# Performance work log

Measured on AMD Instinct MI355X. Metric: run time of the kernel, lower is better.

The kernel has to match this reference:

```python
import jax, jax.numpy as jnp
import numpy as np

N_EMBD = 512
HEAD_SIZE = 64
B, T = 256, 256


def setup_inputs() -> dict:
    key = jax.random.key(0)
    ks = jax.random.split(key, 7)
    s = 1.0 / np.sqrt(N_EMBD)
    return {
        "x": jax.random.normal(ks[0], (B, T, N_EMBD), dtype=jnp.float32),
        "Wk": jax.random.uniform(ks[1], (N_EMBD, HEAD_SIZE), jnp.float32, -s, s),
        "bk": jax.random.uniform(ks[2], (HEAD_SIZE,), jnp.float32, -s, s),
        "Wq": jax.random.uniform(ks[3], (N_EMBD, HEAD_SIZE), jnp.float32, -s, s),
        "bq": jax.random.uniform(ks[4], (HEAD_SIZE,), jnp.float32, -s, s),
        "Wv": jax.random.uniform(ks[5], (N_EMBD, HEAD_SIZE), jnp.float32, -s, s),
        "bv": jax.random.uniform(ks[6], (HEAD_SIZE,), jnp.float32, -s, s),
    }


def reference(x, Wk, bk, Wq, bq, Wv, bv):
    # Single-head causal self-attention (dropout = identity in eval mode).
    Bq, Tq, C = x.shape
    k = x @ Wk + bk        # [B, T, H]
    q = x @ Wq + bq        # [B, T, H]
    v = x @ Wv + bv        # [B, T, H]
    scale = 1.0 / jnp.sqrt(jnp.asarray(k.shape[-1], x.dtype))
    scores = jnp.einsum('bth,bsh->bts', q, k) * scale  # [B, T, T]
    causal = jnp.tril(jnp.ones((Tq, Tq), dtype=bool))
    scores = jnp.where(causal, scores, -jnp.inf)
    attn = jax.nn.softmax(scores, axis=-1)
    return jnp.einsum('bts,bsh->bth', attn, v)  # [B, T, H]
```

## Files before the change

kernel.cpp:

```cpp
#include <hip/hip_runtime.h>
#include <stdint.h>

typedef __attribute__((ext_vector_type(8))) short bf16x8;
typedef __attribute__((ext_vector_type(4))) float f32x4;

#if __has_builtin(__builtin_amdgcn_exp2f)
#define EXP2F(x) __builtin_amdgcn_exp2f(x)
#else
#define EXP2F(x) exp2f(x)
#endif

__device__ __forceinline__ short f2bf(float f) {
    union { float f; uint32_t u; } c; c.f = f;
    return (short)((c.u + 0x7fffu + ((c.u >> 16) & 1u)) >> 16);
}

typedef __attribute__((address_space(1))) void gvoid;
typedef __attribute__((address_space(3))) void lvoid;
__device__ __forceinline__ void async_cp16(const void* g, void* l) {
    __builtin_amdgcn_global_load_lds((gvoid*)g, (lvoid*)l, 16, 0, 0);
}

__global__ void prep_kernel(const float* __restrict__ Wk, const float* __restrict__ bk,
                            const float* __restrict__ Wq, const float* __restrict__ bq,
                            const float* __restrict__ Wv, const float* __restrict__ bv,
                            short* __restrict__ Wt2g, float* __restrict__ bcat) {
    const int col = blockIdx.x;
    const float* W; const float* bb; int c0;
    if (col < 64)       { W = Wk; bb = bk; c0 = col; }
    else if (col < 128) { W = Wq; bb = bq; c0 = col - 64; }
    else                { W = Wv; bb = bv; c0 = col - 128; }
    for (int c = threadIdx.x; c < 512; c += blockDim.x) {
        const int k5 = c & 31;
        Wt2g[(c >> 5) * 6144 + col * 32 + ((((k5 >> 3) ^ (col & 3)) << 3)) + (k5 & 7)] =
            f2bf(W[(size_t)c * 64 + c0]);
    }
    if (threadIdx.x == 0) bcat[col] = bb[c0];
}

#define PSTR 40

__global__ __launch_bounds__(1024, 4) void fused_kernel(
    const float* __restrict__ x, const short* __restrict__ Wt2g,
    const float* __restrict__ bcat, float* __restrict__ out) {
    extern __shared__ __align__(16) char smem[];

    const int tid = threadIdx.x;
    const int wave = tid >> 6, lane = tid & 63;
    const int quad = lane >> 4, l16 = lane & 15;
    const int b = blockIdx.x;
    const int t = wave;

    f32x4 acc[12];
#pragma unroll
    for (int i = 0; i < 12; i++) acc[i] = (f32x4){0.f, 0.f, 0.f, 0.f};

    const int xr = lane >> 3;
    const int xsl = lane & 7;

#define STAGE_X(kc, bufp)                                                           \
    for (int g = 0; g < 2; g++) {                                                   \
        const int i = wave + g * 16;                                                \
        const int r = i * 8 + xr;                                                   \
        const int s = xsl ^ ((r & 3) << 1);                                         \
        async_cp16(x + ((size_t)b * 256 + r) * 512 + (kc) * 32 + s * 4,             \
                   smem + (bufp) * 32768 + i * 1024);                               \
    }
#define STAGE_W(kc, bufp)                                                           \
    if (wave < 12) {                                                                \
        async_cp16(Wt2g + (size_t)(kc) * 6144 + wave * 512 + lane * 8,              \
                   smem + 65536 + (bufp) * 12288 + wave * 1024);                    \
    }

    STAGE_X(0, 0)
    STAGE_W(0, 0)
    __syncthreads();

    const int axoff = (quad ^ (l16 & 3)) * 8;
    const int bxoff = (quad ^ (l16 & 3)) << 3;
    const int arow = t * 16 + l16;
    for (int kc = 0; kc < 16; kc++) {
        const int buf = kc & 1;
        if (kc < 15) { STAGE_X(kc + 1, buf ^ 1) STAGE_W(kc + 1, buf ^ 1) }
        const float* xa = (const float*)(smem + buf * 32768) + arow * 32 + axoff;
        f32x4 u0 = *(const f32x4*)xa, u1 = *(const f32x4*)(xa + 4);
        bf16x8 a;
#pragma unroll
        for (int i = 0; i < 4; i++) { a[i] = f2bf(u0[i]); a[4 + i] = f2bf(u1[i]); }
        const short* wb = (const short*)(smem + 65536 + buf * 12288);
#pragma unroll
        for (int nt = 0; nt < 12; nt++) {
            bf16x8 bfrag = *(const bf16x8*)&wb[(nt * 16 + l16) * 32 + bxoff];
            acc[nt] = __builtin_amdgcn_mfma_f32_16x16x32_bf16(a, bfrag, acc[nt], 0, 0, 0);
        }
        __syncthreads();
    }

    short* Ks  = (short*)smem;
    short* Qs  = (short*)(smem + 32768);
    short* Vts = (short*)(smem + 65536);
    short* Ps  = (short*)(smem + 98304);
#pragma unroll
    for (int nt = 0; nt < 12; nt++) {
        const int col = nt * 16 + l16;
        const float bias = bcat[col];
        const int h = col & 63;
#pragma unroll
        for (int r = 0; r < 4; r++) {
            const short v = f2bf(acc[nt][r] + bias);
            const int row = t * 16 + quad * 4 + r;
            if (nt < 4)
                Ks[row * 64 + (((h >> 3) ^ (row & 7)) << 3) + (h & 7)] = v;
            else if (nt < 8)
                Qs[row * 64 + (((h >> 3) ^ (row & 7)) << 3) + (h & 7)] = v;
            else
                Vts[h * 256 + (((row >> 3) ^ (h & 7)) << 3) + (row & 7)] = v;
        }
    }
    __syncthreads();

    const int qt = ((wave >> 2) << 2) | ((wave & 3) ^ (wave >> 2));
    const float sc2 = 0.125f * 1.44269504088896340736f;
    short* myP = Ps + wave * (16 * PSTR);

    const int qrow = qt * 16 + l16;
    const int sw = l16 & 7;
    bf16x8 qf0 = *(const bf16x8*)&Qs[qrow * 64 + ((quad ^ sw) << 3)];
    bf16x8 qf1 = *(const bf16x8*)&Qs[qrow * 64 + (((4 + quad) ^ sw) << 3)];

    f32x4 St[16];
#pragma unroll
    for (int i = 0; i < 16; i++) St[i] = (f32x4){0.f, 0.f, 0.f, 0.f};
    __builtin_amdgcn_s_setprio(1);
#pragma unroll
    for (int nt = 0; nt < 16; nt++) if (nt <= qt) {
        const int krow = nt * 16 + l16;
        bf16x8 kf0 = *(const bf16x8*)&Ks[krow * 64 + ((quad ^ sw) << 3)];
        bf16x8 kf1 = *(const bf16x8*)&Ks[krow * 64 + (((4 + quad) ^ sw) << 3)];
        St[nt] = __builtin_amdgcn_mfma_f32_16x16x32_bf16(qf0, kf0, St[nt], 0, 0, 0);
        St[nt] = __builtin_amdgcn_mfma_f32_16x16x32_bf16(qf1, kf1, St[nt], 0, 0, 0);
    }
    __builtin_amdgcn_s_setprio(0);

    const int rowq = qt * 16 + quad * 4;
    float mx[4], ls[4];
#pragma unroll
    for (int r = 0; r < 4; r++) mx[r] = -3.0e38f;
#pragma unroll
    for (int nt = 0; nt < 16; nt++) if (nt <= qt) {
        const int cs = nt * 16 + l16;
#pragma unroll
        for (int r = 0; r < 4; r++) {
            float s = (cs <= rowq + r) ? St[nt][r] * sc2 : -3.0e38f;
            St[nt][r] = s;
            mx[r] = fmaxf(mx[r], s);
        }
    }
#pragma unroll
    for (int d = 1; d < 16; d <<= 1)
#pragma unroll
        for (int r = 0; r < 4; r++)
            mx[r] = fmaxf(mx[r], __shfl_xor(mx[r], d, 64));
#pragma unroll
    for (int r = 0; r < 4; r++) ls[r] = 0.f;
#pragma unroll
    for (int nt = 0; nt < 16; nt++) if (nt <= qt) {
#pragma unroll
        for (int r = 0; r < 4; r++) {
            float p = EXP2F(St[nt][r] - mx[r]);
            St[nt][r] = p;
            ls[r] += p;
        }
    }
#pragma unroll
    for (int d = 1; d < 16; d <<= 1)
#pragma unroll
        for (int r = 0; r < 4; r++)
            ls[r] += __shfl_xor(ls[r], d, 64);

    f32x4 O[4];
#pragma unroll
    for (int i = 0; i < 4; i++) O[i] = (f32x4){0.f, 0.f, 0.f, 0.f};
    const int nch = (qt + 2) >> 1;
    __builtin_amdgcn_s_setprio(1);
#pragma unroll
    for (int c2 = 0; c2 < 8; c2++) if (c2 < nch) {
#pragma unroll
        for (int t2i = 0; t2i < 2; t2i++) {
            const int nt = c2 * 2 + t2i;
#pragma unroll
            for (int r = 0; r < 4; r++)
                myP[(quad * 4 + r) * PSTR + t2i * 16 + l16] = f2bf(St[nt][r]);
        }
        bf16x8 pf = *(const bf16x8*)&myP[l16 * PSTR + quad * 8];
#pragma unroll
        for (int ht = 0; ht < 4; ht++) {
            const int h = ht * 16 + l16;
            bf16x8 vf = *(const bf16x8*)&Vts[h * 256 + (((c2 * 4 + quad) ^ (h & 7)) << 3)];
            O[ht] = __builtin_amdgcn_mfma_f32_16x16x32_bf16(pf, vf, O[ht], 0, 0, 0);
        }
    }
    __builtin_amdgcn_s_setprio(0);

    float rls[4];
#pragma unroll
    for (int r = 0; r < 4; r++) rls[r] = 1.0f / ls[r];
#pragma unroll
    for (int ht = 0; ht < 4; ht++)
#pragma unroll
        for (int r = 0; r < 4; r++)
            out[((size_t)b * 256 + rowq + r) * 64 + ht * 16 + l16] = O[ht][r] * rls[r];
#undef STAGE_X
#undef STAGE_W
}

extern "C" void kernel_launch(void* const* d_in, const int* in_sizes, int n_in,
                              void* d_out, int out_size, void* d_ws, size_t ws_size,
                              hipStream_t stream) {
    const float* x  = (const float*)d_in[0];
    const float* Wk = (const float*)d_in[1];
    const float* bk = (const float*)d_in[2];
    const float* Wq = (const float*)d_in[3];
    const float* bq = (const float*)d_in[4];
    const float* Wv = (const float*)d_in[5];
    const float* bv = (const float*)d_in[6];
    float* out = (float*)d_out;

    char* ws = (char*)d_ws;
    short* Wt2g = (short*)(ws);
    float* bcat = (float*)(ws + 196608);

    const int smem_bytes = 118784;
    (void)hipFuncSetAttribute((const void*)fused_kernel,
                              hipFuncAttributeMaxDynamicSharedMemorySize, smem_bytes);

    prep_kernel<<<192, 256, 0, stream>>>(Wk, bk, Wq, bq, Wv, bv, Wt2g, bcat);
    fused_kernel<<<256, 1024, smem_bytes, stream>>>(x, Wt2g, bcat, out);
}
```

Baseline: 217.3 us.

## Split fused projection+attention into separate projection and attention kernels

Moves the QKV projection out of the fused per-batch kernel into its own kernel with 1024 blocks of 256 threads, each handling 64 rows. The projection writes bf16 K, Q and V (V pre-transposed, in the swizzled layout) to a workspace, and the attention kernel bulk-loads them into LDS asynchronously. This aims to raise occupancy and parallelism during the projection GEMM, which previously ran with only 256 large blocks. The cost is an extra global round-trip of about 25 MB of intermediate K/Q/V and one more kernel launch.

```diff
diff --git a/kernel.cpp b/kernel.cpp
--- a/kernel.cpp
+++ b/kernel.cpp
@@ -38,86 +38,125 @@
     if (threadIdx.x == 0) bcat[col] = bb[c0];
 }
 
+__global__ __launch_bounds__(256, 4) void proj_kernel(
+    const float* __restrict__ x, const short* __restrict__ Wt2g,
+    const float* __restrict__ bcat, short* __restrict__ kqv) {
+    __shared__ __align__(16) char smem[40960];
+
+    const int tid = threadIdx.x;
+    const int wave = tid >> 6, lane = tid & 63;
+    const int quad = lane >> 4, l16 = lane & 15;
+    const int blk = blockIdx.x;
+    const int b = blk >> 2, rt = blk & 3;
+    const size_t grow0 = (size_t)blk * 64;
+
+    f32x4 acc[12];
+#pragma unroll
+    for (int i = 0; i < 12; i++) acc[i] = (f32x4){0.f, 0.f, 0.f, 0.f};
+
+    const int xr = lane >> 3;
+    const int xsl = lane & 7;
+
+#define STAGE_X(kc, bufp)                                                           \
+    for (int g = 0; g < 2; g++) {                                                   \
+        const int i = wave + g * 4;                                                 \
+        const int r = i * 8 + xr;                                                   \
+        const int s = xsl ^ ((r & 3) << 1);                                         \
+        async_cp16(x + (grow0 + r) * 512 + (kc) * 32 + s * 4,                       \
+                   smem + (bufp) * 8192 + i * 1024);                                \
+    }
+#define STAGE_W(kc, bufp)                                                           \
+    for (int jj = 0; jj < 3; jj++) {                                                \
+        const int j = wave * 3 + jj;                                                \
+        async_cp16(Wt2g + (size_t)(kc) * 6144 + j * 512 + lane * 8,                 \
+                   smem + 16384 + (bufp) * 12288 + j * 1024);                       \
+    }
+
+    STAGE_X(0, 0)
+    STAGE_W(0, 0)
+    __syncthreads();
+
+    const int axoff = (quad ^ (l16 & 3)) * 8;
+    const int bxoff = (quad ^ (l16 & 3)) << 3;
+    const int arow = wave * 16 + l16;
+    for (int kc = 0; kc < 16; kc++) {
+        const int buf = kc & 1;
+        if (kc < 15) { STAGE_X(kc + 1, buf ^ 1) STAGE_W(kc + 1, buf ^ 1) }
+        const float* xa = (const float*)(smem + buf * 8192) + arow * 32 + axoff;
+        f32x4 u0 = *(const f32x4*)xa, u1 = *(const f32x4*)(xa + 4);
+        bf16x8 a;
+#pragma unroll
+        for (int i = 0; i < 4; i++) { a[i] = f2bf(u0[i]); a[4 + i] = f2bf(u1[i]); }
+        const short* wb = (const short*)(smem + 16384 + buf * 12288);
+#pragma unroll
+        for (int nt = 0; nt < 12; nt++) {
+            bf16x8 bfrag = *(const bf16x8*)&wb[(nt * 16 + l16) * 32 + bxoff];
+            acc[nt] = __builtin_amdgcn_mfma_f32_16x16x32_bf16(a, bfrag, acc[nt], 0, 0, 0);
+        }
+        __syncthreads();
+    }
+
+    short* Kl = (short*)smem;
+    short* Ql = (short*)(smem + 8192);
+    short* Vl = (short*)(smem + 16384);
+#pragma unroll
+    for (int nt = 0; nt < 12; nt++) {
+        const int col = nt * 16 + l16;
+        const float bias = bcat[col];
+        const int h = col & 63;
+#pragma unroll
+        for (int r = 0; r < 4; r++) {
+            const short v = f2bf(acc[nt][r] + bias);
+            const int lrow = wave * 16 + quad * 4 + r;
+            if (nt < 4)
+                Kl[lrow * 64 + (((h >> 3) ^ (lrow & 7)) << 3) + (h & 7)] = v;
+            else if (nt < 8)
+                Ql[lrow * 64 + (((h >> 3) ^ (lrow & 7)) << 3) + (h & 7)] = v;
+            else
+                Vl[h * 64 + (((lrow >> 3) ^ (h & 7)) << 3) + (lrow & 7)] = v;
+        }
+    }
+    __syncthreads();
+
+    short* Kg = kqv + (size_t)b * 49152;
+    short* Qg = Kg + 16384;
+    short* Vg = Kg + 32768;
+#pragma unroll
+    for (int it = 0; it < 2; it++) {
+        const int vi = tid + it * 256;
+        ((f32x4*)(Kg + rt * 4096))[vi] = ((const f32x4*)Kl)[vi];
+        ((f32x4*)(Qg + rt * 4096))[vi] = ((const f32x4*)Ql)[vi];
+        const int h = vi >> 3, wi = vi & 7;
+        *(f32x4*)(Vg + h * 256 + rt * 64 + wi * 8) = ((const f32x4*)Vl)[vi];
+    }
+#undef STAGE_X
+#undef STAGE_W
+}
+
 #define PSTR 40
 
-__global__ __launch_bounds__(1024, 4) void fused_kernel(
-    const float* __restrict__ x, const short* __restrict__ Wt2g,
-    const float* __restrict__ bcat, float* __restrict__ out) {
+__global__ __launch_bounds__(1024, 4) void attn_kernel(
+    const short* __restrict__ kqv, float* __restrict__ out) {
     extern __shared__ __align__(16) char smem[];
 
     const int tid = threadIdx.x;
     const int wave = tid >> 6, lane = tid & 63;
     const int quad = lane >> 4, l16 = lane & 15;
     const int b = blockIdx.x;
-    const int t = wave;
-
-    f32x4 acc[12];
-#pragma unroll
-    for (int i = 0; i < 12; i++) acc[i] = (f32x4){0.f, 0.f, 0.f, 0.f};
-
-    const int xr = lane >> 3;
-    const int xsl = lane & 7;
-
-#define STAGE_X(kc, bufp)                                                           \
-    for (int g = 0; g < 2; g++) {                                                   \
-        const int i = wave + g * 16;                                                \
-        const int r = i * 8 + xr;                                                   \
-        const int s = xsl ^ ((r & 3) << 1);                                         \
-        async_cp16(x + ((size_t)b * 256 + r) * 512 + (kc) * 32 + s * 4,             \
-                   smem + (bufp) * 32768 + i * 1024);                               \
-    }
-#define STAGE_W(kc, bufp)                                                           \
-    if (wave < 12) {                                                                \
-        async_cp16(Wt2g + (size_t)(kc) * 6144 + wave * 512 + lane * 8,              \
-                   smem + 65536 + (bufp) * 12288 + wave * 1024);                    \
-    }
-
-    STAGE_X(0, 0)
-    STAGE_W(0, 0)
+
+    const short* kqvb = kqv + (size_t)b * 49152;
+#pragma unroll
+    for (int gg = 0; gg < 6; gg++) {
+        const int G = wave + gg * 16;
+        async_cp16(kqvb + G * 512 + lane * 8, smem + G * 1024);
+    }
+    asm volatile("s_waitcnt vmcnt(0)" ::: "memory");
     __syncthreads();
-
-    const int axoff = (quad ^ (l16 & 3)) * 8;
-    const int bxoff = (quad ^ (l16 & 3)) << 3;
-    const int arow = t * 16 + l16;
-    for (int kc = 0; kc < 16; kc++) {
-        const int buf = kc & 1;
-        if (kc < 15) { STAGE_X(kc + 1, buf ^ 1) STAGE_W(kc + 1, buf ^ 1) }
-        const float* xa = (const float*)(smem + buf * 32768) + arow * 32 + axoff;
-        f32x4 u0 = *(const f32x4*)xa, u1 = *(const f32x4*)(xa + 4);
-        bf16x8 a;
-#pragma unroll
-        for (int i = 0; i < 4; i++) { a[i] = f2bf(u0[i]); a[4 + i] = f2bf(u1[i]); }
-        const short* wb = (const short*)(smem + 65536 + buf * 12288);
-#pragma unroll
-        for (int nt = 0; nt < 12; nt++) {
-            bf16x8 bfrag = *(const bf16x8*)&wb[(nt * 16 + l16) * 32 + bxoff];
-            acc[nt] = __builtin_amdgcn_mfma_f32_16x16x32_bf16(a, bfrag, acc[nt], 0, 0, 0);
-        }
-        __syncthreads();
-    }
 
     short* Ks  = (short*)smem;
     short* Qs  = (short*)(smem + 32768);
     short* Vts = (short*)(smem + 65536);
     short* Ps  = (short*)(smem + 98304);
-#pragma unroll
-    for (int nt = 0; nt < 12; nt++) {
-        const int col = nt * 16 + l16;
-        const float bias = bcat[col];
-        const int h = col & 63;
-#pragma unroll
-        for (int r = 0; r < 4; r++) {
-            const short v = f2bf(acc[nt][r] + bias);
-            const int row = t * 16 + quad * 4 + r;
-            if (nt < 4)
-                Ks[row * 64 + (((h >> 3) ^ (row & 7)) << 3) + (h & 7)] = v;
-            else if (nt < 8)
-                Qs[row * 64 + (((h >> 3) ^ (row & 7)) << 3) + (h & 7)] = v;
-            else
-                Vts[h * 256 + (((row >> 3) ^ (h & 7)) << 3) + (row & 7)] = v;
-        }
-    }
-    __syncthreads();
 
     const int qt = ((wave >> 2) << 2) | ((wave & 3) ^ (wave >> 2));
     const float sc2 = 0.125f * 1.44269504088896340736f;
@@ -210,8 +249,6 @@
 #pragma unroll
         for (int r = 0; r < 4; r++)
             out[((size_t)b * 256 + rowq + r) * 64 + ht * 16 + l16] = O[ht][r] * rls[r];
-#undef STAGE_X
-#undef STAGE_W
 }
 
 extern "C" void kernel_launch(void* const* d_in, const int* in_sizes, int n_in,
@@ -229,11 +266,13 @@
     char* ws = (char*)d_ws;
     short* Wt2g = (short*)(ws);
     float* bcat = (float*)(ws + 196608);
+    short* kqv  = (short*)(ws + 262144);
 
     const int smem_bytes = 118784;
-    (void)hipFuncSetAttribute((const void*)fused_kernel,
+    (void)hipFuncSetAttribute((const void*)attn_kernel,
                               hipFuncAttributeMaxDynamicSharedMemorySize, smem_bytes);
 
     prep_kernel<<<192, 256, 0, stream>>>(Wk, bk, Wq, bq, Wv, bv, Wt2g, bcat);
-    fused_kernel<<<256, 1024, smem_bytes, stream>>>(x, Wt2g, bcat, out);
-}
+    proj_kernel<<<1024, 256, 0, stream>>>(x, Wt2g, bcat, kqv);
+    attn_kernel<<<256, 1024, smem_bytes, stream>>>(kqv, out);
+}
```

New measurement: 224.2 us. +3.2%, slower.
